# Performance work log

Measured on AMD Instinct MI355X. Metric: run time of the kernel, lower is better.

## Reference

```python
import jax, jax.numpy as jnp
import numpy as np

N_NODES = 50000
N_EDGES = 1_600_000
NUM_GRAPHS = 64
F_NODE = 32
F_EDGE = 16
H = 64
L = 3
BN_EPS = 1e-5


def setup_inputs() -> dict:
    key = jax.random.key(0)
    ks = jax.random.split(key, 20)
    x = jax.random.normal(ks[0], (N_NODES, F_NODE), jnp.float32)
    edge_attr = jax.random.normal(ks[1], (N_EDGES, F_EDGE), jnp.float32)
    edge_index = jax.random.randint(ks[2], (2, N_EDGES), 0, N_NODES, dtype=jnp.int64)
    batch = jnp.sort(jax.random.randint(ks[3], (N_NODES,), 0, NUM_GRAPHS, dtype=jnp.int64))

    def lin(k, fan_in, shape):
        return jax.random.normal(k, shape, jnp.float32) * (1.0 / np.sqrt(fan_in))

    node_W = lin(ks[4], F_NODE, (F_NODE, H));  node_b = jnp.zeros((H,), jnp.float32)
    edge_W = lin(ks[5], F_EDGE, (F_EDGE, H));  edge_b = jnp.zeros((H,), jnp.float32)
    # GINE per-layer MLP: Linear(H, 2H) -> ReLU -> Linear(2H, H)
    W1s = lin(ks[6], H, (L, H, 2 * H));   b1s = jnp.zeros((L, 2 * H), jnp.float32)
    W2s = lin(ks[7], 2 * H, (L, 2 * H, H)); b2s = jnp.zeros((L, H), jnp.float32)
    gammas = jnp.ones((L, H), jnp.float32)
    betas = jnp.zeros((L, H), jnp.float32)
    lin_W = lin(ks[8], H, (H, 1));  lin_b = jnp.zeros((1,), jnp.float32)
    return {
        "x": x, "edge_attr": edge_attr, "edge_index": edge_index, "batch": batch,
        "node_W": node_W, "node_b": node_b, "edge_W": edge_W, "edge_b": edge_b,
        "W1s": W1s, "b1s": b1s, "W2s": W2s, "b2s": b2s,
        "gammas": gammas, "betas": betas, "lin_W": lin_W, "lin_b": lin_b,
    }


def reference(x, edge_attr, edge_index, batch, node_W, node_b, edge_W, edge_b,
              W1s, b1s, W2s, b2s, gammas, betas, lin_W, lin_b):
    # node / edge embeddings
    h = x @ node_W + node_b                  # [N, H]
    e = edge_attr @ edge_W + edge_b          # [E, H]
    src, dst = edge_index[0], edge_index[1]
    for l in range(L):
        # GINEConv (eps=0): m_ij = relu(x_j + e_ij), aggregate sum at target
        m = jax.nn.relu(h[src] + e)                                  # [E, H]
        agg = jax.ops.segment_sum(m, dst, num_segments=N_NODES)     # [N, H]
        z = h + agg
        z = jax.nn.relu(z @ W1s[l] + b1s[l]) @ W2s[l] + b2s[l]       # GINE MLP
        # BatchNorm (training-mode batch stats, biased variance) + ReLU
        mu = jnp.mean(z, axis=0)
        var = jnp.var(z, axis=0)
        h = jax.nn.relu(gammas[l] * (z - mu) * jax.lax.rsqrt(var + BN_EPS) + betas[l])
    # global mean pool per graph
    counts = jax.ops.segment_sum(jnp.ones((N_NODES,), h.dtype), batch, num_segments=NUM_GRAPHS)
    gsum = jax.ops.segment_sum(h, batch, num_segments=NUM_GRAPHS)   # [G, H]
    graph_x = gsum / jnp.maximum(counts, 1.0)[:, None]
    return graph_x @ lin_W + lin_b                                   # [G, 1]
```

## Files before the change

kernel.cpp:

```cpp
#include <hip/hip_runtime.h>

#define NN 50000
#define NE 1600000
#define NG 64
#define HD 64
#define BN_EPS 1e-5f
#define NTILES ((NN + 31) / 32)

typedef unsigned short ushort_t;
typedef unsigned int uint_t;
typedef __attribute__((ext_vector_type(8))) short bf16x8;
typedef __attribute__((ext_vector_type(4))) float f32x4;

__device__ __forceinline__ float b2f(ushort_t u) {
  union { uint_t i; float f; } v; v.i = ((uint_t)u) << 16; return v.f;
}
__device__ __forceinline__ ushort_t f2b(float f) {
  union { float f; uint_t i; } v; v.f = f;
  uint_t x = v.i;
  return (ushort_t)((x + 0x7fffu + ((x >> 16) & 1u)) >> 16);
}
__device__ __forceinline__ uint_t packsplit(float f) {
  ushort_t hi = f2b(f);
  float r = f - b2f(hi);
  ushort_t lo = f2b(r);
  return (uint_t)hi | ((uint_t)lo << 16);
}
__device__ __forceinline__ float LDF(const void* p, int i, int isb) {
  return isb ? b2f(((const ushort_t*)p)[i]) : ((const float*)p)[i];
}
__device__ __forceinline__ int LDI(const void* p, int i, int is64) {
  return is64 ? ((const int*)p)[2 * i] : ((const int*)p)[i];
}
__device__ __forceinline__ int clampi(int v, int hi) {
  return (v < 0) ? 0 : (v >= hi ? hi - 1 : v);
}

__global__ void detect_k(const uint_t* __restrict__ xw, const uint_t* __restrict__ ew,
                         int* __restrict__ flags) {
  int t = threadIdx.x;
  uint_t w = xw[t];
  uint_t b = (w >> 8) & 0x7fu;
  unsigned long long m1 = __ballot(b >= 0x3au && b <= 0x42u);
  unsigned long long m2 = __ballot(ew[2 * t + 1] == 0u);
  if (t == 0) {
    flags[0] = (__popcll(m1) >= 32) ? 1 : 0;
    flags[1] = (__popcll(m2) >= 56) ? 1 : 0;
  }
}

__global__ void __launch_bounds__(256) node_embed(
    const void* __restrict__ x, const void* __restrict__ W,
    const void* __restrict__ b, float* __restrict__ h, const int* __restrict__ flags) {
  __shared__ float xs[64 * 32];
  int isb = flags[0];
  int t = threadIdx.x;
  int base = blockIdx.x * 64;
  int nodes = NN - base; if (nodes > 64) nodes = 64;
  int idx = t * 8;
  if (idx < nodes * 32) {
    if (isb) {
      const uint4* p = (const uint4*)((const ushort_t*)x + base * 32);
      uint4 u = p[t];
      ushort_t* pu = (ushort_t*)&u;
      #pragma unroll
      for (int q = 0; q < 8; q++) xs[idx + q] = b2f(pu[q]);
    } else {
      const float4* p = (const float4*)((const float*)x + base * 32);
      float4 a = p[2 * t], d = p[2 * t + 1];
      xs[idx + 0] = a.x; xs[idx + 1] = a.y; xs[idx + 2] = a.z; xs[idx + 3] = a.w;
      xs[idx + 4] = d.x; xs[idx + 5] = d.y; xs[idx + 6] = d.z; xs[idx + 7] = d.w;
    }
  }
  int c = t & 63, s0 = t >> 6;
  float w[32];
  #pragma unroll
  for (int k = 0; k < 32; k++) w[k] = LDF(W, k * 64 + c, isb);
  float bc = LDF(b, c, isb);
  __syncthreads();
  #pragma unroll 4
  for (int i = 0; i < 16; i++) {
    int slot = s0 * 16 + i;
    int node = base + slot;
    if (node < NN) {
      float acc = bc;
      #pragma unroll
      for (int k = 0; k < 32; k++) acc += xs[slot * 32 + k] * w[k];
      h[node * 64 + c] = acc;
    }
  }
}

__global__ void __launch_bounds__(256) hist_k(
    const void* __restrict__ eidx, int* __restrict__ hist, const int* __restrict__ flags) {
  int is64 = flags[1];
  int e = blockIdx.x * 256 + threadIdx.x;
  if (e >= NE) return;
  int d = clampi(LDI(eidx, NE + e, is64), NN);
  atomicAdd(&hist[d], 1);
}

__global__ void __launch_bounds__(1024) scan_k(
    const int* __restrict__ hist, int* __restrict__ offs) {
  __shared__ int buf[1024];
  int t = threadIdx.x;
  int beg = t * 49, end = beg + 49; if (end > NN) end = NN; if (beg > NN) beg = NN;
  int s = 0;
  for (int i = beg; i < end; i++) s += hist[i];
  buf[t] = s;
  __syncthreads();
  for (int d = 1; d < 1024; d <<= 1) {
    int x = (t >= d) ? buf[t - d] : 0;
    __syncthreads();
    buf[t] += x;
    __syncthreads();
  }
  int run = buf[t] - s;
  for (int i = beg; i < end; i++) { int hv = hist[i]; offs[i] = run; run += hv; }
  if (t == 1023) offs[NN] = run;
}

__global__ void __launch_bounds__(256) scatter_k(
    const void* __restrict__ eidx, int* __restrict__ cursor,
    int* __restrict__ perm, int* __restrict__ psrc, int* __restrict__ pdst,
    const int* __restrict__ flags) {
  int is64 = flags[1];
  int e = blockIdx.x * 256 + threadIdx.x;
  if (e >= NE) return;
  int d = clampi(LDI(eidx, NE + e, is64), NN);
  int s = clampi(LDI(eidx, e, is64), NN);
  int pos = atomicAdd(&cursor[d], 1);
  perm[pos] = e;
  psrc[pos] = s;
  pdst[pos] = d;
}

__global__ void __launch_bounds__(256) edge_sorted(
    const void* __restrict__ eattr, const int* __restrict__ perm,
    const int* __restrict__ psrc, const int* __restrict__ pdst,
    const void* __restrict__ eW, const void* __restrict__ eb,
    const float* __restrict__ h, float* __restrict__ agg, const int* __restrict__ flags) {
  __shared__ float ea[64 * 16];
  __shared__ int ss[64], sd[64];
  int isb = flags[0];
  int t = threadIdx.x;
  int base = blockIdx.x * 64;
  if (t < 64) ss[t] = psrc[base + t];
  else if (t < 128) sd[t - 64] = pdst[base + t - 64];
  {
    int slot = t >> 2, q = t & 3;
    int pe = perm[base + slot];
    if (isb) {
      const uint2* p = (const uint2*)((const ushort_t*)eattr + (size_t)pe * 16 + q * 4);
      uint2 u = *p;
      ea[slot * 16 + q * 4 + 0] = b2f((ushort_t)(u.x & 0xffffu));
      ea[slot * 16 + q * 4 + 1] = b2f((ushort_t)(u.x >> 16));
      ea[slot * 16 + q * 4 + 2] = b2f((ushort_t)(u.y & 0xffffu));
      ea[slot * 16 + q * 4 + 3] = b2f((ushort_t)(u.y >> 16));
    } else {
      const float4* p = (const float4*)((const float*)eattr + (size_t)pe * 16 + q * 4);
      float4 v = *p;
      ea[slot * 16 + q * 4 + 0] = v.x;
      ea[slot * 16 + q * 4 + 1] = v.y;
      ea[slot * 16 + q * 4 + 2] = v.z;
      ea[slot * 16 + q * 4 + 3] = v.w;
    }
  }
  int c = t & 63, s0 = t >> 6;
  float w[16];
  #pragma unroll
  for (int k = 0; k < 16; k++) w[k] = LDF(eW, k * 64 + c, isb);
  float bc = LDF(eb, c, isb);
  __syncthreads();
  float acc = 0.f;
  int cur = -1;
  for (int i = 0; i < 16; i++) {
    int slot = s0 * 16 + i;
    int sn = ss[slot], dn = sd[slot];
    float e = bc;
    #pragma unroll
    for (int k = 0; k < 16; k++) e += ea[slot * 16 + k] * w[k];
    float m = h[sn * 64 + c] + e;
    m = m > 0.f ? m : 0.f;
    if (dn != cur) {
      if (cur >= 0) atomicAdd(&agg[cur * 64 + c], acc);
      cur = dn; acc = 0.f;
    }
    acc += m;
  }
  if (cur >= 0) atomicAdd(&agg[cur * 64 + c], acc);
}

__global__ void __launch_bounds__(256) prep_w(
    const void* __restrict__ W1s, const void* __restrict__ W2s,
    uint4* __restrict__ wpk, const int* __restrict__ flags) {
  int l = blockIdx.x, t = threadIdx.x, isb = flags[0];
  uint4* w1hi = wpk + (size_t)l * 4096;
  uint4* w1lo = w1hi + 1024;
  uint4* w2hi = w1hi + 2048;
  uint4* w2lo = w1hi + 3072;
  union U8 { ushort_t s[8]; uint4 u; };
  for (int o = t; o < 1024; o += 256) {
    int lane = o & 63, f = (o >> 6) & 7, hh = o >> 9;
    int q = lane >> 4, m = lane & 15;
    {
      int kc = f >> 2, i = f & 3;
      U8 hi, lo;
      #pragma unroll
      for (int j = 0; j < 8; j++) {
        int idx = l * 8192 + (kc * 32 + q * 8 + j) * 128 + (hh * 4 + i) * 16 + m;
        float wf = LDF(W1s, idx, isb);
        ushort_t hb = f2b(wf);
        hi.s[j] = hb;
        lo.s[j] = f2b(wf - b2f(hb));
      }
      w1hi[o] = hi.u;
      w1lo[o] = lo.u;
    }
    {
      int kc = f >> 1, i = f & 1;
      U8 hi, lo;
      #pragma unroll
      for (int j = 0; j < 8; j++) {
        int idx = l * 8192 + (kc * 32 + q * 8 + j) * 64 + (hh * 2 + i) * 16 + m;
        float wf = LDF(W2s, idx, isb);
        ushort_t hb = f2b(wf);
        hi.s[j] = hb;
        lo.s[j] = f2b(wf - b2f(hb));
      }
      w2hi[o] = hi.u;
      w2lo[o] = lo.u;
    }
  }
}

__global__ void __launch_bounds__(256) mlp_mfma(
    const float* __restrict__ h, const float* agg,
    const uint4* __restrict__ wpk, const void* __restrict__ b1s,
    const void* __restrict__ b2s,
    float* z2out, float* __restrict__ bnsum, const int* __restrict__ flags, int layer) {
  __shared__ uint_t zs[32 * 65];
  __shared__ uint_t a1s[32 * 129];
  int isb = flags[0];
  int t = threadIdx.x;
  int w = t >> 6, lane = t & 63, q = lane >> 4, m = lane & 15;
  int mt = w & 1;
  int hh = w >> 1;
  int ng1 = hh * 4;
  int ng2 = hh * 2;
  int b1off = layer * 128, b2off = layer * 64;
  const uint4* w1hi = wpk + (size_t)layer * 4096;
  const uint4* w1lo = w1hi + 1024;
  const uint4* w2hi = w1hi + 2048;
  const uint4* w2lo = w1hi + 3072;

  union FR { uint4 u; bf16x8 v; };
  FR w1f[4][2], w2f[2][4];
  #pragma unroll
  for (int kc = 0; kc < 2; kc++)
    #pragma unroll
    for (int i = 0; i < 4; i++)
      w1f[i][kc].u = w1hi[(hh * 8 + kc * 4 + i) * 64 + lane];
  #pragma unroll
  for (int kc = 0; kc < 4; kc++)
    #pragma unroll
    for (int i = 0; i < 2; i++)
      w2f[i][kc].u = w2hi[(hh * 8 + kc * 2 + i) * 64 + lane];

  float b1v[4], b2v[2];
  #pragma unroll
  for (int i = 0; i < 4; i++) b1v[i] = LDF(b1s, b1off + (ng1 + i) * 16 + m, isb);
  #pragma unroll
  for (int i = 0; i < 2; i++) b2v[i] = LDF(b2s, b2off + (ng2 + i) * 16 + m, isb);

  int srow = t >> 3, scol = (t & 7) * 8;
  float ps[2] = {0.f, 0.f}, pq[2] = {0.f, 0.f};

  for (int tile = blockIdx.x; tile < NTILES; tile += gridDim.x) {
    int base = tile * 32;
    __syncthreads();
    {
      int gr = base + srow;
      if (gr < NN) {
        const float4* hp = (const float4*)(h + (size_t)gr * 64 + scol);
        const float4* ap = (const float4*)(agg + (size_t)gr * 64 + scol);
        float4 h0 = hp[0], h1 = hp[1], a0 = ap[0], a1 = ap[1];
        zs[srow * 65 + scol + 0] = packsplit(h0.x + a0.x);
        zs[srow * 65 + scol + 1] = packsplit(h0.y + a0.y);
        zs[srow * 65 + scol + 2] = packsplit(h0.z + a0.z);
        zs[srow * 65 + scol + 3] = packsplit(h0.w + a0.w);
        zs[srow * 65 + scol + 4] = packsplit(h1.x + a1.x);
        zs[srow * 65 + scol + 5] = packsplit(h1.y + a1.y);
        zs[srow * 65 + scol + 6] = packsplit(h1.z + a1.z);
        zs[srow * 65 + scol + 7] = packsplit(h1.w + a1.w);
      } else {
        #pragma unroll
        for (int jj = 0; jj < 8; jj++) zs[srow * 65 + scol + jj] = 0;
      }
    }
    __syncthreads();
    f32x4 acc1[4];
    #pragma unroll
    for (int i = 0; i < 4; i++) acc1[i] = (f32x4){0.f, 0.f, 0.f, 0.f};
    #pragma unroll
    for (int kc = 0; kc < 2; kc++) {
      int ab = (mt * 16 + m) * 65 + kc * 32 + q * 8;
      bf16x8 ahi, alo;
      #pragma unroll
      for (int j = 0; j < 8; j++) {
        uint_t u = zs[ab + j];
        ahi[j] = (short)(u & 0xffffu);
        alo[j] = (short)(u >> 16);
      }
      #pragma unroll
      for (int i = 0; i < 4; i++) {
        acc1[i] = __builtin_amdgcn_mfma_f32_16x16x32_bf16(ahi, w1f[i][kc].v, acc1[i], 0, 0, 0);
        acc1[i] = __builtin_amdgcn_mfma_f32_16x16x32_bf16(alo, w1f[i][kc].v, acc1[i], 0, 0, 0);
        if (!isb) {
          FR bl;
          bl.u = w1lo[(hh * 8 + kc * 4 + i) * 64 + lane];
          acc1[i] = __builtin_amdgcn_mfma_f32_16x16x32_bf16(ahi, bl.v, acc1[i], 0, 0, 0);
        }
      }
    }
    #pragma unroll
    for (int i = 0; i < 4; i++) {
      #pragma unroll
      for (int r = 0; r < 4; r++) {
        float v = acc1[i][r] + b1v[i];
        v = v > 0.f ? v : 0.f;
        a1s[(mt * 16 + q * 4 + r) * 129 + (ng1 + i) * 16 + m] = packsplit(v);
      }
    }
    __syncthreads();
    f32x4 acc2[2];
    #pragma unroll
    for (int i = 0; i < 2; i++) acc2[i] = (f32x4){0.f, 0.f, 0.f, 0.f};
    #pragma unroll
    for (int kc = 0; kc < 4; kc++) {
      int ab = (mt * 16 + m) * 129 + kc * 32 + q * 8;
      bf16x8 ahi, alo;
      #pragma unroll
      for (int j = 0; j < 8; j++) {
        uint_t u = a1s[ab + j];
        ahi[j] = (short)(u & 0xffffu);
        alo[j] = (short)(u >> 16);
      }
      #pragma unroll
      for (int i = 0; i < 2; i++) {
        acc2[i] = __builtin_amdgcn_mfma_f32_16x16x32_bf16(ahi, w2f[i][kc].v, acc2[i], 0, 0, 0);
        acc2[i] = __builtin_amdgcn_mfma_f32_16x16x32_bf16(alo, w2f[i][kc].v, acc2[i], 0, 0, 0);
        if (!isb) {
          FR bl;
          bl.u = w2lo[(hh * 8 + kc * 2 + i) * 64 + lane];
          acc2[i] = __builtin_amdgcn_mfma_f32_16x16x32_bf16(ahi, bl.v, acc2[i], 0, 0, 0);
        }
      }
    }
    #pragma unroll
    for (int i = 0; i < 2; i++) {
      int col = (ng2 + i) * 16 + m;
      #pragma unroll
      for (int r = 0; r < 4; r++) {
        int gr = base + mt * 16 + q * 4 + r;
        if (gr < NN) {
          float v = acc2[i][r] + b2v[i];
          z2out[(size_t)gr * 64 + col] = v;
          ps[i] += v; pq[i] += v * v;
        }
      }
    }
  }
  __syncthreads();
  float* red = (float*)zs;
  if (t < 128) red[t] = 0.f;
  __syncthreads();
  #pragma unroll
  for (int i = 0; i < 2; i++) {
    int col = (ng2 + i) * 16 + m;
    atomicAdd(&red[col], ps[i]);
    atomicAdd(&red[64 + col], pq[i]);
  }
  __syncthreads();
  if (t < 128) atomicAdd(&bnsum[t], red[t]);
}

__global__ void bn_fin(const float* __restrict__ bnsum, const void* __restrict__ gammas,
                       const void* __restrict__ betas, float* __restrict__ scsh,
                       const int* __restrict__ flags, int layer) {
  int c = threadIdx.x;
  int isb = flags[0];
  float inv_n = 1.0f / (float)NN;
  float mu = bnsum[c] * inv_n;
  float var = bnsum[64 + c] * inv_n - mu * mu;
  var = var > 0.f ? var : 0.f;
  float sc = LDF(gammas, layer * 64 + c, isb) * rsqrtf(var + BN_EPS);
  scsh[c] = sc;
  scsh[64 + c] = LDF(betas, layer * 64 + c, isb) - mu * sc;
}

__global__ void __launch_bounds__(256) bn_apply(
    const float* __restrict__ z2, const float* __restrict__ scsh, float* __restrict__ h) {
  int t = blockIdx.x * 256 + threadIdx.x;
  if (t < NN * 16) {
    float4 z = ((const float4*)z2)[t];
    int c4 = t & 15;
    float4 sc = ((const float4*)scsh)[c4];
    float4 sh = ((const float4*)(scsh + 64))[c4];
    float4 r;
    r.x = fmaxf(z.x * sc.x + sh.x, 0.f);
    r.y = fmaxf(z.y * sc.y + sh.y, 0.f);
    r.z = fmaxf(z.z * sc.z + sh.z, 0.f);
    r.w = fmaxf(z.w * sc.w + sh.w, 0.f);
    ((float4*)h)[t] = r;
  }
}

__global__ void __launch_bounds__(256) find_bounds(
    const void* __restrict__ batch, int* __restrict__ bounds, const int* __restrict__ flags) {
  int is64 = flags[1];
  int i = blockIdx.x * 256 + threadIdx.x;
  if (i >= NN) return;
  int cur = clampi(LDI(batch, i, is64), NG);
  if (i == 0) {
    for (int g = 0; g <= cur; g++) bounds[g] = 0;
  } else {
    int prev = clampi(LDI(batch, i - 1, is64), NG);
    for (int g = prev + 1; g <= cur; g++) bounds[g] = i;
  }
  if (i == NN - 1) {
    for (int g = cur + 1; g <= NG; g++) bounds[g] = NN;
  }
}

__global__ void __launch_bounds__(256) pool_final(
    const float* __restrict__ h, const int* __restrict__ bounds,
    const void* __restrict__ linW, const void* __restrict__ linB,
    float* __restrict__ out, const int* __restrict__ flags) {
  __shared__ float red[4][64];
  int isb = flags[0];
  int g = blockIdx.x;
  int t = threadIdx.x, c = t & 63, w = t >> 6;
  int s = bounds[g], e = bounds[g + 1];
  float acc = 0.f;
  for (int i = s + w; i < e; i += 4) acc += h[i * 64 + c];
  red[w][c] = acc;
  __syncthreads();
  if (t < 64) {
    float v = red[0][c] + red[1][c] + red[2][c] + red[3][c];
    float cnt = (float)(e - s); if (cnt < 1.f) cnt = 1.f;
    v = (v / cnt) * LDF(linW, c, isb);
    #pragma unroll
    for (int m = 32; m >= 1; m >>= 1) v += __shfl_xor(v, m, 64);
    if (c == 0) out[g] = v + LDF(linB, 0, isb);
  }
}

extern "C" void kernel_launch(void* const* d_in, const int* in_sizes, int n_in,
                              void* d_out, int out_size, void* d_ws, size_t ws_size,
                              hipStream_t stream) {
  const void* x     = d_in[0];
  const void* eattr = d_in[1];
  const void* eidx  = d_in[2];
  const void* batch = d_in[3];
  const void* nodeW = d_in[4];
  const void* nodeB = d_in[5];
  const void* edgeW = d_in[6];
  const void* edgeB = d_in[7];
  const void* W1s   = d_in[8];
  const void* b1s   = d_in[9];
  const void* W2s   = d_in[10];
  const void* b2s   = d_in[11];
  const void* gam   = d_in[12];
  const void* bet   = d_in[13];
  const void* linW  = d_in[14];
  const void* linB  = d_in[15];
  float* out = (float*)d_out;

  int*   flags  = (int*)d_ws;
  float* h      = (float*)d_ws + 16;
  float* agg    = h + (size_t)NN * HD;
  float* bnsum  = agg + (size_t)NN * HD;
  float* scsh   = bnsum + 128;
  int*   bounds = (int*)(scsh + 128);
  int*   offs   = bounds + 80;
  int*   cursor = offs + (NN + 1);
  int*   perm   = cursor + (NN + 1);
  int*   psrc   = perm + NE;
  int*   pdst   = psrc + NE;

  size_t base_words = 16ull + 2ull * NN * HD + 128 + 128 + 80;
  size_t sort_words = base_words + 2ull * (NN + 1) + 3ull * NE;
  size_t wpk_words_start = (sort_words + 3ull) & ~3ull;
  size_t wpk_words = 3ull * 4096 * 4;
  size_t needed = (wpk_words_start + wpk_words) * 4ull;
  if (ws_size < needed) return;
  uint4* wpk = (uint4*)((float*)d_ws + wpk_words_start);
  float* z2sep = (float*)d_ws + wpk_words_start + wpk_words;
  float* z2 = (ws_size >= (wpk_words_start + wpk_words + (size_t)NN * HD) * 4ull)
                  ? z2sep : agg;

  detect_k<<<1, 64, 0, stream>>>((const uint_t*)x, (const uint_t*)eidx, flags);
  prep_w<<<3, 256, 0, stream>>>(W1s, W2s, wpk, flags);
  node_embed<<<(NN + 63) / 64, 256, 0, stream>>>(x, nodeW, nodeB, h, flags);

  hipMemsetAsync(offs, 0, (NN + 1) * sizeof(int), stream);
  hist_k<<<NE / 256, 256, 0, stream>>>(eidx, offs, flags);
  scan_k<<<1, 1024, 0, stream>>>(offs, cursor);
  scatter_k<<<NE / 256, 256, 0, stream>>>(eidx, cursor, perm, psrc, pdst, flags);

  for (int l = 0; l < 3; l++) {
    hipMemsetAsync(agg, 0, (size_t)NN * HD * sizeof(float), stream);
    edge_sorted<<<NE / 64, 256, 0, stream>>>(eattr, perm, psrc, pdst, edgeW, edgeB, h, agg, flags);
    hipMemsetAsync(bnsum, 0, 128 * sizeof(float), stream);
    mlp_mfma<<<784, 256, 0, stream>>>(h, agg, wpk, b1s, b2s, z2, bnsum, flags, l);
    bn_fin<<<1, 64, 0, stream>>>(bnsum, gam, bet, scsh, flags, l);
    bn_apply<<<3125, 256, 0, stream>>>(z2, scsh, h);
  }
  find_bounds<<<(NN + 255) / 256, 256, 0, stream>>>(batch, bounds, flags);
  pool_final<<<NG, 256, 0, stream>>>(h, bounds, linW, linB, out, flags);
}
```

Baseline: 958.0 us.

## Pre-permute edge attributes during scatter and compute edge embedding with MFMA

The scatter step now writes the edge attributes in dst-sorted order as packed bf16 hi/lo pairs, together with packed (src,dst) int2 indices, so the per-layer edge kernel reads them contiguously instead of gathering through perm. The new edge kernel computes the 16->64 edge embedding with split-bf16 MFMA and then does a per-destination run-length accumulation before each atomic. This costs extra workspace (16 words per edge) and a larger one-time scatter, and it falls back to the old path when the workspace is too small.

```diff
diff --git a/kernel.cpp b/kernel.cpp
--- a/kernel.cpp
+++ b/kernel.cpp
@@ -120,6 +120,39 @@
   if (t == 1023) offs[NN] = run;
 }
 
+__global__ void __launch_bounds__(256) scatter_fused(
+    const void* __restrict__ eidx, const void* __restrict__ eattr,
+    int* __restrict__ cursor, int2* __restrict__ pidx, uint_t* __restrict__ eap,
+    const int* __restrict__ flags) {
+  int isb = flags[0], is64 = flags[1];
+  int e = blockIdx.x * 256 + threadIdx.x;
+  if (e >= NE) return;
+  int d = clampi(LDI(eidx, NE + e, is64), NN);
+  int s = clampi(LDI(eidx, e, is64), NN);
+  int pos = atomicAdd(&cursor[d], 1);
+  pidx[pos] = make_int2(s, d);
+  uint_t wbuf[16];
+  if (isb) {
+    const uint4* p = (const uint4*)((const ushort_t*)eattr + (size_t)e * 16);
+    uint4 a = p[0], b = p[1];
+    const ushort_t* pv = (const ushort_t*)&a;
+    #pragma unroll
+    for (int j = 0; j < 8; j++) wbuf[j] = (uint_t)pv[j];
+    const ushort_t* pv2 = (const ushort_t*)&b;
+    #pragma unroll
+    for (int j = 0; j < 8; j++) wbuf[8 + j] = (uint_t)pv2[j];
+  } else {
+    const float* p = (const float*)eattr + (size_t)e * 16;
+    #pragma unroll
+    for (int j = 0; j < 16; j++) wbuf[j] = packsplit(p[j]);
+  }
+  uint4* dst = (uint4*)(eap + (size_t)pos * 16);
+  dst[0] = make_uint4(wbuf[0], wbuf[1], wbuf[2], wbuf[3]);
+  dst[1] = make_uint4(wbuf[4], wbuf[5], wbuf[6], wbuf[7]);
+  dst[2] = make_uint4(wbuf[8], wbuf[9], wbuf[10], wbuf[11]);
+  dst[3] = make_uint4(wbuf[12], wbuf[13], wbuf[14], wbuf[15]);
+}
+
 __global__ void __launch_bounds__(256) scatter_k(
     const void* __restrict__ eidx, int* __restrict__ cursor,
     int* __restrict__ perm, int* __restrict__ psrc, int* __restrict__ pdst,
@@ -133,6 +166,83 @@
   perm[pos] = e;
   psrc[pos] = s;
   pdst[pos] = d;
+}
+
+__global__ void __launch_bounds__(256) edge_mfma(
+    const uint_t* __restrict__ eap, const int2* __restrict__ pidx,
+    const void* __restrict__ eW, const void* __restrict__ eb,
+    const float* __restrict__ h, float* __restrict__ agg, const int* __restrict__ flags) {
+  __shared__ float ebuf[4 * 1088];
+  __shared__ int ss[64], sd[64];
+  int isb = flags[0];
+  int t = threadIdx.x;
+  int w = t >> 6, lane = t & 63, q = lane >> 4, m = lane & 15;
+  int base = blockIdx.x * 64;
+  if (t < 64) {
+    int2 v = pidx[base + t];
+    ss[t] = v.x; sd[t] = v.y;
+  }
+  bf16x8 ah, al;
+  #pragma unroll
+  for (int j = 0; j < 8; j++) { ah[j] = 0; al[j] = 0; }
+  if (q < 2) {
+    const uint4* ap = (const uint4*)(eap + (size_t)(base + w * 16 + m) * 16 + q * 8);
+    uint4 u0 = ap[0], u1 = ap[1];
+    uint_t uu[8] = {u0.x, u0.y, u0.z, u0.w, u1.x, u1.y, u1.z, u1.w};
+    #pragma unroll
+    for (int j = 0; j < 8; j++) {
+      ah[j] = (short)(uu[j] & 0xffffu);
+      al[j] = (short)(uu[j] >> 16);
+    }
+  }
+  bf16x8 bh[4], bl[4];
+  #pragma unroll
+  for (int i = 0; i < 4; i++) {
+    #pragma unroll
+    for (int j = 0; j < 8; j++) {
+      int k = q * 8 + j;
+      float wf = (k < 16) ? LDF(eW, k * 64 + i * 16 + m, isb) : 0.f;
+      ushort_t hb = f2b(wf);
+      bh[i][j] = (short)hb;
+      bl[i][j] = (short)f2b(wf - b2f(hb));
+    }
+  }
+  float ebv[4];
+  #pragma unroll
+  for (int i = 0; i < 4; i++) ebv[i] = LDF(eb, i * 16 + m, isb);
+  f32x4 acc[4];
+  #pragma unroll
+  for (int i = 0; i < 4; i++) acc[i] = (f32x4){0.f, 0.f, 0.f, 0.f};
+  #pragma unroll
+  for (int i = 0; i < 4; i++) {
+    acc[i] = __builtin_amdgcn_mfma_f32_16x16x32_bf16(ah, bh[i], acc[i], 0, 0, 0);
+    if (!isb) {
+      acc[i] = __builtin_amdgcn_mfma_f32_16x16x32_bf16(al, bh[i], acc[i], 0, 0, 0);
+      acc[i] = __builtin_amdgcn_mfma_f32_16x16x32_bf16(ah, bl[i], acc[i], 0, 0, 0);
+    }
+  }
+  #pragma unroll
+  for (int i = 0; i < 4; i++)
+    #pragma unroll
+    for (int r = 0; r < 4; r++)
+      ebuf[w * 1088 + (q * 4 + r) * 68 + i * 16 + m] = acc[i][r] + ebv[i];
+  __syncthreads();
+  int c = t & 63;
+  float racc = 0.f;
+  int cur = -1;
+  for (int i = 0; i < 16; i++) {
+    int slot = w * 16 + i;
+    int sn = ss[slot], dn = sd[slot];
+    float e = ebuf[w * 1088 + i * 68 + c];
+    float mv = h[sn * 64 + c] + e;
+    mv = mv > 0.f ? mv : 0.f;
+    if (dn != cur) {
+      if (cur >= 0) atomicAdd(&agg[cur * 64 + c], racc);
+      cur = dn; racc = 0.f;
+    }
+    racc += mv;
+  }
+  if (cur >= 0) atomicAdd(&agg[cur * 64 + c], racc);
 }
 
 __global__ void __launch_bounds__(256) edge_sorted(
@@ -485,20 +595,32 @@
   int*   bounds = (int*)(scsh + 128);
   int*   offs   = bounds + 80;
   int*   cursor = offs + (NN + 1);
-  int*   perm   = cursor + (NN + 1);
-  int*   psrc   = perm + NE;
-  int*   pdst   = psrc + NE;
 
   size_t base_words = 16ull + 2ull * NN * HD + 128 + 128 + 80;
-  size_t sort_words = base_words + 2ull * (NN + 1) + 3ull * NE;
-  size_t wpk_words_start = (sort_words + 3ull) & ~3ull;
-  size_t wpk_words = 3ull * 4096 * 4;
-  size_t needed = (wpk_words_start + wpk_words) * 4ull;
-  if (ws_size < needed) return;
-  uint4* wpk = (uint4*)((float*)d_ws + wpk_words_start);
-  float* z2sep = (float*)d_ws + wpk_words_start + wpk_words;
-  float* z2 = (ws_size >= (wpk_words_start + wpk_words + (size_t)NN * HD) * 4ull)
-                  ? z2sep : agg;
+  size_t oc_end     = base_words + 2ull * (NN + 1);
+  size_t reg_start  = (oc_end + 15ull) & ~15ull;
+  size_t wpk_words  = 3ull * 4096 * 4;
+
+  size_t eap_off  = reg_start;
+  size_t pidx_off = eap_off + 16ull * NE;
+  size_t wpk_new  = (pidx_off + 2ull * NE + 3ull) & ~3ull;
+  size_t end_new  = wpk_new + wpk_words;
+  size_t perm_off = reg_start;
+  size_t wpk_old  = (perm_off + 3ull * NE + 3ull) & ~3ull;
+  size_t end_old  = wpk_old + wpk_words;
+
+  bool big = ws_size >= end_new * 4ull;
+  if (!big && ws_size < end_old * 4ull) return;
+
+  float* wsf = (float*)d_ws;
+  uint_t* eap  = (uint_t*)(wsf + eap_off);
+  int2*   pidx = (int2*)(wsf + pidx_off);
+  int*    perm = (int*)(wsf + perm_off);
+  int*    psrc = perm + NE;
+  int*    pdst = psrc + NE;
+  uint4*  wpk  = (uint4*)(wsf + (big ? wpk_new : wpk_old));
+  size_t  endw = big ? end_new : end_old;
+  float*  z2   = (ws_size >= (endw + (size_t)NN * HD) * 4ull) ? (wsf + endw) : agg;
 
   detect_k<<<1, 64, 0, stream>>>((const uint_t*)x, (const uint_t*)eidx, flags);
   prep_w<<<3, 256, 0, stream>>>(W1s, W2s, wpk, flags);
@@ -507,11 +629,17 @@
   hipMemsetAsync(offs, 0, (NN + 1) * sizeof(int), stream);
   hist_k<<<NE / 256, 256, 0, stream>>>(eidx, offs, flags);
   scan_k<<<1, 1024, 0, stream>>>(offs, cursor);
-  scatter_k<<<NE / 256, 256, 0, stream>>>(eidx, cursor, perm, psrc, pdst, flags);
+  if (big)
+    scatter_fused<<<NE / 256, 256, 0, stream>>>(eidx, eattr, cursor, pidx, eap, flags);
+  else
+    scatter_k<<<NE / 256, 256, 0, stream>>>(eidx, cursor, perm, psrc, pdst, flags);
 
   for (int l = 0; l < 3; l++) {
     hipMemsetAsync(agg, 0, (size_t)NN * HD * sizeof(float), stream);
-    edge_sorted<<<NE / 64, 256, 0, stream>>>(eattr, perm, psrc, pdst, edgeW, edgeB, h, agg, flags);
+    if (big)
+      edge_mfma<<<NE / 64, 256, 0, stream>>>(eap, pidx, edgeW, edgeB, h, agg, flags);
+    else
+      edge_sorted<<<NE / 64, 256, 0, stream>>>(eattr, perm, psrc, pdst, edgeW, edgeB, h, agg, flags);
     hipMemsetAsync(bnsum, 0, 128 * sizeof(float), stream);
     mlp_mfma<<<784, 256, 0, stream>>>(h, agg, wpk, b1s, b2s, z2, bnsum, flags, l);
     bn_fin<<<1, 64, 0, stream>>>(bnsum, gam, bet, scsh, flags, l);
```

Measured after the change: 1.038 ms. 8.4% more time.
